# Kernel tuning notes

Hardware: AMD Instinct MI355X
Metric: run time of the kernel (lower is better)

The kernel has to match this reference:

```python
import jax, jax.numpy as jnp
import numpy as np
import itertools

B, G, FEAT, IMG = 2048, 8, 512, 1024
SCALES = list(range(G, 1, -1))  # [8,7,6,5,4,3,2]
SUBSAMPLE = 12


def setup_inputs() -> dict:
    key = jax.random.key(0)
    keys = jax.random.split(key, 1 + 2 * len(SCALES))
    rng = np.random.default_rng(0)
    inp = {"input": jax.random.normal(keys[0], (B, G, FEAT), dtype=jnp.float32)}
    for i, scale in enumerate(SCALES):
        perms = np.array(list(itertools.permutations(range(G), scale)), dtype=np.int32)
        n_sub = min(SUBSAMPLE, len(perms))
        sel = rng.choice(len(perms), n_sub, replace=False)
        inp[f"perms{i}"] = jnp.asarray(perms[sel])  # [n_sub, scale] int32
        lim = 1.0 / np.sqrt(scale * FEAT)
        inp[f"W{i}"] = jax.random.uniform(keys[1 + 2 * i], (IMG, scale * FEAT), minval=-lim, maxval=lim, dtype=jnp.float32)
        inp[f"b{i}"] = jax.random.uniform(keys[2 + 2 * i], (IMG,), minval=-lim, maxval=lim, dtype=jnp.float32)
    return inp


def _forward(input, perms_list, W_list, b_list):
    outs = []
    for perms, W, b in zip(perms_list, W_list, b_list):
        # gather: [B, n_sub, scale, FEAT] -> [B, n_sub, scale*FEAT]
        g = input[:, perms, :]
        g = g.reshape(g.shape[0], g.shape[1], -1)
        # batched linear over all subsamples, then mean over subsamples
        y = jnp.einsum('bsf,df->bsd', g, W) + b  # [B, n_sub, IMG]
        outs.append(y.mean(axis=1))
    return jnp.concatenate(outs, axis=1)  # [B, len(SCALES)*IMG]


def reference(input, perms0, W0, b0, perms1, W1, b1, perms2, W2, b2,
              perms3, W3, b3, perms4, W4, b4, perms5, W5, b5, perms6, W6, b6):
    perms_list = [perms0, perms1, perms2, perms3, perms4, perms5, perms6]
    W_list = [W0, W1, W2, W3, W4, W5, W6]
    b_list = [b0, b1, b2, b3, b4, b5, b6]
    return _forward(input, perms_list, W_list, b_list)
```

## Files before the change

kernel.cpp:

```cpp
#include <hip/hip_runtime.h>

typedef unsigned short u16;
typedef __bf16 bf16x8 __attribute__((ext_vector_type(8)));
typedef float f32x4 __attribute__((ext_vector_type(4)));

__device__ __forceinline__ u16 f2bf(float f) {
  unsigned int u = __float_as_uint(f);
  return (u16)((u + 0x7fffu + ((u >> 16) & 1u)) >> 16);
}

__device__ __forceinline__ int cumK(int i) { return 256 * i * (17 - i); }

__global__ __launch_bounds__(256) void k_xbar(
    const float* __restrict__ x,
    const int* p0, const int* p1, const int* p2, const int* p3,
    const int* p4, const int* p5, const int* p6,
    u16* __restrict__ Xb) {
  __shared__ float sc[448];
  const int b = blockIdx.x;
  const int t = threadIdx.x;
  const int* ps[7] = {p0, p1, p2, p3, p4, p5, p6};
  for (int cell = t; cell < 448; cell += 256) {
    int i = cell >> 6, rem = cell & 63, g = rem >> 3, j = rem & 7;
    int scale = 8 - i;
    float v = 0.f;
    if (j < scale) {
      const int* p = ps[i];
      int cnt = 0;
      for (int s = 0; s < 12; ++s) cnt += (p[s * scale + j] == g) ? 1 : 0;
      v = (float)cnt * (1.0f / 12.0f);
    }
    sc[cell] = v;
  }
  __syncthreads();
  const int u = t & 63;
  const int wv = t >> 6;
  const float4* xrow = reinterpret_cast<const float4*>(x + (size_t)b * 4096);
  float4 xr0[8], xr1[8];
#pragma unroll
  for (int g = 0; g < 8; ++g) {
    xr0[g] = xrow[g * 128 + u * 2];
    xr1[g] = xrow[g * 128 + u * 2 + 1];
  }
  u16* orow = Xb + (size_t)b * 17920;
  for (int s = wv; s < 35; s += 4) {
    int i = 0, rem = s;
    while (rem >= 8 - i) { rem -= 8 - i; ++i; }
    const int j = rem;
    float4 A0 = make_float4(0.f, 0.f, 0.f, 0.f);
    float4 A1 = make_float4(0.f, 0.f, 0.f, 0.f);
#pragma unroll
    for (int g = 0; g < 8; ++g) {
      const float c = sc[i * 64 + g * 8 + j];
      A0.x += c * xr0[g].x; A0.y += c * xr0[g].y;
      A0.z += c * xr0[g].z; A0.w += c * xr0[g].w;
      A1.x += c * xr1[g].x; A1.y += c * xr1[g].y;
      A1.z += c * xr1[g].z; A1.w += c * xr1[g].w;
    }
    uint4 o;
    o.x = (unsigned)f2bf(A0.x) | ((unsigned)f2bf(A0.y) << 16);
    o.y = (unsigned)f2bf(A0.z) | ((unsigned)f2bf(A0.w) << 16);
    o.z = (unsigned)f2bf(A1.x) | ((unsigned)f2bf(A1.y) << 16);
    o.w = (unsigned)f2bf(A1.z) | ((unsigned)f2bf(A1.w) << 16);
    *reinterpret_cast<uint4*>(orow + cumK(i) + j * 512 + u * 8) = o;
  }
}

__global__ __launch_bounds__(256) void k_wcast(
    const float* W0, const float* W1, const float* W2, const float* W3,
    const float* W4, const float* W5, const float* W6,
    u16* __restrict__ Wcat) {
  int i = 0, rem = blockIdx.x;
  while (rem >= (8 - i) * 512) { rem -= (8 - i) * 512; ++i; }
  const float* Wi = (i == 0) ? W0 : (i == 1) ? W1 : (i == 2) ? W2 :
                    (i == 3) ? W3 : (i == 4) ? W4 : (i == 5) ? W5 : W6;
  const int t = threadIdx.x;
  const float4 w = reinterpret_cast<const float4*>(Wi)[(size_t)rem * 256 + t];
  ushort4 o;
  o.x = f2bf(w.x); o.y = f2bf(w.y); o.z = f2bf(w.z); o.w = f2bf(w.w);
  reinterpret_cast<ushort4*>(Wcat + ((size_t)cumK(i) + rem) * 1024)[t] = o;
}

__device__ __forceinline__ void gl_lds16(const u16* g, u16* l) {
  __builtin_amdgcn_global_load_lds(
      (const __attribute__((address_space(1))) void*)g,
      (__attribute__((address_space(3))) void*)l, 16, 0, 0);
}

#define WAIT_VM8 0x0F78
#define WAIT_VM0 0x0F70

__global__ __launch_bounds__(256) void k_gemm_ms(
    const u16* __restrict__ Xb, const u16* __restrict__ Wcat,
    const float* b0, const float* b1, const float* b2, const float* b3,
    const float* b4, const float* b5, const float* b6,
    float* __restrict__ out) {
  __shared__ u16 lds[2 * 16384];
  const int i = blockIdx.x >> 7;
  const int s = blockIdx.x & 127;
  const int region = s & 7;
  const int k = s >> 3;
  const int mq = region >> 1;
  const int nq = region & 1;
  const int m0 = (mq * 4 + (k & 3)) * 128;
  const int n0loc = (nq * 4 + (k >> 2)) * 128;
  const int K = (8 - i) * 512;
  const int niter = K >> 6;
  const size_t baseB = (size_t)cumK(i) * 1024;

  const int tid = threadIdx.x;
  const int lane = tid & 63;
  const int wave = tid >> 6;
  const int quad = lane >> 4;
  const int l15 = lane & 15;
  const int waveM = (wave >> 1) * 64;
  const int waveN = (wave & 1) * 64;

  const int srow = tid >> 3;
  const int sslot = tid & 7;
  const int gch = (sslot - srow) & 7;
  const u16* pA0 = Xb + (size_t)(m0 + srow) * 17920 + cumK(i) + gch * 8;
  const u16* pB0 = Wcat + baseB + (size_t)(n0loc + srow) * K + gch * 8;
  const size_t strideAj = (size_t)32 * 17920;
  const size_t strideBj = (size_t)32 * K;
  u16* lA0 = lds + tid * 8;
  u16* lB0 = lds + 8192 + tid * 8;

  int offA[2][4], offB[2][4];
#pragma unroll
  for (int t = 0; t < 2; ++t) {
#pragma unroll
    for (int q = 0; q < 4; ++q) {
      int rowA = waveM + q * 16 + l15;
      offA[t][q] = rowA * 64 + (((t * 4 + quad) + rowA) & 7) * 8;
      int rowB = waveN + q * 16 + l15;
      offB[t][q] = 8192 + rowB * 64 + (((t * 4 + quad) + rowB) & 7) * 8;
    }
  }

  f32x4 acc[4][4];
#pragma unroll
  for (int q = 0; q < 4; ++q)
#pragma unroll
    for (int c = 0; c < 4; ++c) {
      f32x4 z = {0.f, 0.f, 0.f, 0.f};
      acc[q][c] = z;
    }

#pragma unroll
  for (int j = 0; j < 4; ++j) {
    gl_lds16(pA0 + j * strideAj, lA0 + j * 2048);
    gl_lds16(pB0 + j * strideBj, lB0 + j * 2048);
  }

  for (int kt = 0; kt < niter - 1; ++kt) {
    const size_t ko = (size_t)(kt + 1) * 64;
    const int nb = ((kt + 1) & 1) << 14;
#pragma unroll
    for (int j = 0; j < 4; ++j) {
      gl_lds16(pA0 + j * strideAj + ko, lA0 + nb + j * 2048);
      gl_lds16(pB0 + j * strideBj + ko, lB0 + nb + j * 2048);
    }
    __builtin_amdgcn_s_waitcnt(WAIT_VM8);
    __builtin_amdgcn_s_barrier();
    const int boff = (kt & 1) << 14;
#pragma unroll
    for (int t = 0; t < 2; ++t) {
      bf16x8 av[4], bv[4];
#pragma unroll
      for (int q = 0; q < 4; ++q) av[q] = *reinterpret_cast<const bf16x8*>(lds + boff + offA[t][q]);
#pragma unroll
      for (int c = 0; c < 4; ++c) bv[c] = *reinterpret_cast<const bf16x8*>(lds + boff + offB[t][c]);
#pragma unroll
      for (int q = 0; q < 4; ++q)
#pragma unroll
        for (int c = 0; c < 4; ++c)
          acc[q][c] = __builtin_amdgcn_mfma_f32_16x16x32_bf16(av[q], bv[c], acc[q][c], 0, 0, 0);
    }
    __builtin_amdgcn_s_barrier();
  }

  __builtin_amdgcn_s_waitcnt(WAIT_VM0);
  __builtin_amdgcn_s_barrier();
  {
    const int boff = ((niter - 1) & 1) << 14;
#pragma unroll
    for (int t = 0; t < 2; ++t) {
      bf16x8 av[4], bv[4];
#pragma unroll
      for (int q = 0; q < 4; ++q) av[q] = *reinterpret_cast<const bf16x8*>(lds + boff + offA[t][q]);
#pragma unroll
      for (int c = 0; c < 4; ++c) bv[c] = *reinterpret_cast<const bf16x8*>(lds + boff + offB[t][c]);
#pragma unroll
      for (int q = 0; q < 4; ++q)
#pragma unroll
        for (int c = 0; c < 4; ++c)
          acc[q][c] = __builtin_amdgcn_mfma_f32_16x16x32_bf16(av[q], bv[c], acc[q][c], 0, 0, 0);
    }
  }

  const float* bi = (i == 0) ? b0 : (i == 1) ? b1 : (i == 2) ? b2 :
                    (i == 3) ? b3 : (i == 4) ? b4 : (i == 5) ? b5 : b6;
#pragma unroll
  for (int c = 0; c < 4; ++c) {
    const int nloc = n0loc + waveN + c * 16 + l15;
    const float bias = bi[nloc];
    const int ncol = i * 1024 + nloc;
#pragma unroll
    for (int q = 0; q < 4; ++q) {
      const int mbase = m0 + waveM + q * 16 + quad * 4;
#pragma unroll
      for (int reg = 0; reg < 4; ++reg)
        out[(size_t)(mbase + reg) * 7168 + ncol] = acc[q][c][reg] + bias;
    }
  }
}

extern "C" void kernel_launch(void* const* d_in, const int* in_sizes, int n_in,
                              void* d_out, int out_size, void* d_ws, size_t ws_size,
                              hipStream_t stream) {
  const float* input = (const float*)d_in[0];
  const int* perms[7];
  const float* W[7];
  const float* bias[7];
  for (int i = 0; i < 7; ++i) {
    perms[i] = (const int*)d_in[1 + 3 * i];
    W[i]     = (const float*)d_in[2 + 3 * i];
    bias[i]  = (const float*)d_in[3 + 3 * i];
  }
  char* ws = (char*)d_ws;
  u16* Xb   = (u16*)ws;
  u16* Wcat = (u16*)(ws + (size_t)2048 * 17920 * 2);

  k_xbar<<<2048, 256, 0, stream>>>(input, perms[0], perms[1], perms[2], perms[3],
                                   perms[4], perms[5], perms[6], Xb);
  k_wcast<<<17920, 256, 0, stream>>>(W[0], W[1], W[2], W[3], W[4], W[5], W[6], Wcat);
  k_gemm_ms<<<896, 256, 0, stream>>>(Xb, Wcat,
                                     bias[0], bias[1], bias[2], bias[3],
                                     bias[4], bias[5], bias[6],
                                     (float*)d_out);
}
```

Before: 279.0 us.

## Halve GEMM K-tile to 32 to shrink LDS and raise occupancy; reorder scale blocks

The GEMM K-step drops from 64 to 32, which halves the LDS buffers from 64KB to 32KB and comes with a new 4-chunk swizzle for the shared-memory layout. launch_bounds now asks for 5 blocks per CU so more workgroups can be resident at once. Block-to-scale mapping is also reordered so long-K and short-K scales interleave across the grid, which is meant to balance load. The cost is twice as many barriers and waits per unit of K, with less MFMA work between each sync.

```diff
diff --git a/kernel.cpp b/kernel.cpp
--- a/kernel.cpp
+++ b/kernel.cpp
@@ -87,16 +87,18 @@
       (__attribute__((address_space(3))) void*)l, 16, 0, 0);
 }
 
-#define WAIT_VM8 0x0F78
+#define WAIT_VM4 0x0F74
 #define WAIT_VM0 0x0F70
 
-__global__ __launch_bounds__(256) void k_gemm_ms(
+__global__ __launch_bounds__(256, 5) void k_gemm_ms(
     const u16* __restrict__ Xb, const u16* __restrict__ Wcat,
     const float* b0, const float* b1, const float* b2, const float* b3,
     const float* b4, const float* b5, const float* b6,
     float* __restrict__ out) {
-  __shared__ u16 lds[2 * 16384];
-  const int i = blockIdx.x >> 7;
+  __shared__ u16 lds[2 * 8192];
+  const int r = blockIdx.x >> 7;
+  const int i = (r == 0) ? 0 : (r == 1) ? 1 : (r == 2) ? 4 :
+                (r == 3) ? 2 : (r == 4) ? 5 : (r == 5) ? 3 : 6;
   const int s = blockIdx.x & 127;
   const int region = s & 7;
   const int k = s >> 3;
@@ -105,7 +107,7 @@
   const int m0 = (mq * 4 + (k & 3)) * 128;
   const int n0loc = (nq * 4 + (k >> 2)) * 128;
   const int K = (8 - i) * 512;
-  const int niter = K >> 6;
+  const int niter = K >> 5;
   const size_t baseB = (size_t)cumK(i) * 1024;
 
   const int tid = threadIdx.x;
@@ -116,26 +118,22 @@
   const int waveM = (wave >> 1) * 64;
   const int waveN = (wave & 1) * 64;
 
-  const int srow = tid >> 3;
-  const int sslot = tid & 7;
-  const int gch = (sslot - srow) & 7;
+  const int srow = tid >> 2;
+  const int gch = ((tid & 3) - (tid >> 3)) & 3;
   const u16* pA0 = Xb + (size_t)(m0 + srow) * 17920 + cumK(i) + gch * 8;
   const u16* pB0 = Wcat + baseB + (size_t)(n0loc + srow) * K + gch * 8;
-  const size_t strideAj = (size_t)32 * 17920;
-  const size_t strideBj = (size_t)32 * K;
+  const size_t strideA2 = (size_t)64 * 17920;
+  const size_t strideB2 = (size_t)64 * K;
   u16* lA0 = lds + tid * 8;
-  u16* lB0 = lds + 8192 + tid * 8;
-
-  int offA[2][4], offB[2][4];
-#pragma unroll
-  for (int t = 0; t < 2; ++t) {
-#pragma unroll
-    for (int q = 0; q < 4; ++q) {
-      int rowA = waveM + q * 16 + l15;
-      offA[t][q] = rowA * 64 + (((t * 4 + quad) + rowA) & 7) * 8;
-      int rowB = waveN + q * 16 + l15;
-      offB[t][q] = 8192 + rowB * 64 + (((t * 4 + quad) + rowB) & 7) * 8;
-    }
+  u16* lB0 = lds + 4096 + tid * 8;
+
+  int offA[4], offB[4];
+#pragma unroll
+  for (int q = 0; q < 4; ++q) {
+    int rowA = waveM + q * 16 + l15;
+    offA[q] = rowA * 32 + ((quad + (rowA >> 1)) & 3) * 8;
+    int rowB = waveN + q * 16 + l15;
+    offB[q] = 4096 + rowB * 32 + ((quad + (rowB >> 1)) & 3) * 8;
   }
 
   f32x4 acc[4][4];
@@ -147,56 +145,48 @@
       acc[q][c] = z;
     }
 
-#pragma unroll
-  for (int j = 0; j < 4; ++j) {
-    gl_lds16(pA0 + j * strideAj, lA0 + j * 2048);
-    gl_lds16(pB0 + j * strideBj, lB0 + j * 2048);
-  }
+  gl_lds16(pA0, lA0);
+  gl_lds16(pA0 + strideA2, lA0 + 2048);
+  gl_lds16(pB0, lB0);
+  gl_lds16(pB0 + strideB2, lB0 + 2048);
 
   for (int kt = 0; kt < niter - 1; ++kt) {
-    const size_t ko = (size_t)(kt + 1) * 64;
-    const int nb = ((kt + 1) & 1) << 14;
-#pragma unroll
-    for (int j = 0; j < 4; ++j) {
-      gl_lds16(pA0 + j * strideAj + ko, lA0 + nb + j * 2048);
-      gl_lds16(pB0 + j * strideBj + ko, lB0 + nb + j * 2048);
-    }
-    __builtin_amdgcn_s_waitcnt(WAIT_VM8);
+    const size_t ko = (size_t)(kt + 1) * 32;
+    const int nb = ((kt + 1) & 1) << 13;
+    gl_lds16(pA0 + ko, lA0 + nb);
+    gl_lds16(pA0 + strideA2 + ko, lA0 + nb + 2048);
+    gl_lds16(pB0 + ko, lB0 + nb);
+    gl_lds16(pB0 + strideB2 + ko, lB0 + nb + 2048);
+    __builtin_amdgcn_s_waitcnt(WAIT_VM4);
     __builtin_amdgcn_s_barrier();
-    const int boff = (kt & 1) << 14;
-#pragma unroll
-    for (int t = 0; t < 2; ++t) {
-      bf16x8 av[4], bv[4];
-#pragma unroll
-      for (int q = 0; q < 4; ++q) av[q] = *reinterpret_cast<const bf16x8*>(lds + boff + offA[t][q]);
-#pragma unroll
-      for (int c = 0; c < 4; ++c) bv[c] = *reinterpret_cast<const bf16x8*>(lds + boff + offB[t][c]);
-#pragma unroll
-      for (int q = 0; q < 4; ++q)
-#pragma unroll
-        for (int c = 0; c < 4; ++c)
-          acc[q][c] = __builtin_amdgcn_mfma_f32_16x16x32_bf16(av[q], bv[c], acc[q][c], 0, 0, 0);
-    }
+    const int boff = (kt & 1) << 13;
+    bf16x8 av[4], bv[4];
+#pragma unroll
+    for (int q = 0; q < 4; ++q) av[q] = *reinterpret_cast<const bf16x8*>(lds + boff + offA[q]);
+#pragma unroll
+    for (int c = 0; c < 4; ++c) bv[c] = *reinterpret_cast<const bf16x8*>(lds + boff + offB[c]);
+#pragma unroll
+    for (int q = 0; q < 4; ++q)
+#pragma unroll
+      for (int c = 0; c < 4; ++c)
+        acc[q][c] = __builtin_amdgcn_mfma_f32_16x16x32_bf16(av[q], bv[c], acc[q][c], 0, 0, 0);
     __builtin_amdgcn_s_barrier();
   }
 
   __builtin_amdgcn_s_waitcnt(WAIT_VM0);
   __builtin_amdgcn_s_barrier();
   {
-    const int boff = ((niter - 1) & 1) << 14;
-#pragma unroll
-    for (int t = 0; t < 2; ++t) {
-      bf16x8 av[4], bv[4];
-#pragma unroll
-      for (int q = 0; q < 4; ++q) av[q] = *reinterpret_cast<const bf16x8*>(lds + boff + offA[t][q]);
-#pragma unroll
-      for (int c = 0; c < 4; ++c) bv[c] = *reinterpret_cast<const bf16x8*>(lds + boff + offB[t][c]);
-#pragma unroll
-      for (int q = 0; q < 4; ++q)
-#pragma unroll
-        for (int c = 0; c < 4; ++c)
-          acc[q][c] = __builtin_amdgcn_mfma_f32_16x16x32_bf16(av[q], bv[c], acc[q][c], 0, 0, 0);
-    }
+    const int boff = ((niter - 1) & 1) << 13;
+    bf16x8 av[4], bv[4];
+#pragma unroll
+    for (int q = 0; q < 4; ++q) av[q] = *reinterpret_cast<const bf16x8*>(lds + boff + offA[q]);
+#pragma unroll
+    for (int c = 0; c < 4; ++c) bv[c] = *reinterpret_cast<const bf16x8*>(lds + boff + offB[c]);
+#pragma unroll
+    for (int q = 0; q < 4; ++q)
+#pragma unroll
+      for (int c = 0; c < 4; ++c)
+        acc[q][c] = __builtin_amdgcn_mfma_f32_16x16x32_bf16(av[q], bv[c], acc[q][c], 0, 0, 0);
   }
 
   const float* bi = (i == 0) ? b0 : (i == 1) ? b1 : (i == 2) ? b2 :
```

Measured after the change: 305.2 us. 9.4% more time.

## Switch GEMM to 32x32x16 MFMA tiles and interleave scale block order

Applied to the files above, without the earlier changes.

Replaces the 16x16x32 bf16 MFMA tiling (a 4x4 grid of fragments per wave) with 32x32x16 MFMA (2x2 fragments per wave). This halves the LDS fragment reads per k-step and uses the larger matrix instruction, which has higher operand reuse. It also remaps block index to scale index so long-K and short-K scales are interleaved across the grid, which should balance the tail. The epilogue is rewritten for the 32x32 accumulator layout, and any mistake in the row/column mapping would give wrong outputs.

```diff
diff --git a/kernel.cpp b/kernel.cpp
--- a/kernel.cpp
+++ b/kernel.cpp
@@ -2,7 +2,7 @@
 
 typedef unsigned short u16;
 typedef __bf16 bf16x8 __attribute__((ext_vector_type(8)));
-typedef float f32x4 __attribute__((ext_vector_type(4)));
+typedef float f32x16 __attribute__((ext_vector_type(16)));
 
 __device__ __forceinline__ u16 f2bf(float f) {
   unsigned int u = __float_as_uint(f);
@@ -96,7 +96,9 @@
     const float* b4, const float* b5, const float* b6,
     float* __restrict__ out) {
   __shared__ u16 lds[2 * 16384];
-  const int i = blockIdx.x >> 7;
+  const int r = blockIdx.x >> 7;
+  const int i = (r == 0) ? 0 : (r == 1) ? 1 : (r == 2) ? 4 :
+                (r == 3) ? 2 : (r == 4) ? 5 : (r == 5) ? 3 : 6;
   const int s = blockIdx.x & 127;
   const int region = s & 7;
   const int k = s >> 3;
@@ -111,8 +113,8 @@
   const int tid = threadIdx.x;
   const int lane = tid & 63;
   const int wave = tid >> 6;
-  const int quad = lane >> 4;
-  const int l15 = lane & 15;
+  const int l31 = lane & 31;
+  const int half = lane >> 5;
   const int waveM = (wave >> 1) * 64;
   const int waveN = (wave & 1) * 64;
 
@@ -126,26 +128,24 @@
   u16* lA0 = lds + tid * 8;
   u16* lB0 = lds + 8192 + tid * 8;
 
-  int offA[2][4], offB[2][4];
-#pragma unroll
-  for (int t = 0; t < 2; ++t) {
-#pragma unroll
-    for (int q = 0; q < 4; ++q) {
-      int rowA = waveM + q * 16 + l15;
-      offA[t][q] = rowA * 64 + (((t * 4 + quad) + rowA) & 7) * 8;
-      int rowB = waveN + q * 16 + l15;
-      offB[t][q] = 8192 + rowB * 64 + (((t * 4 + quad) + rowB) & 7) * 8;
-    }
-  }
-
-  f32x4 acc[4][4];
-#pragma unroll
-  for (int q = 0; q < 4; ++q)
-#pragma unroll
-    for (int c = 0; c < 4; ++c) {
-      f32x4 z = {0.f, 0.f, 0.f, 0.f};
-      acc[q][c] = z;
-    }
+  int offA[4][2], offB[4][2];
+#pragma unroll
+  for (int kk = 0; kk < 4; ++kk) {
+#pragma unroll
+    for (int f = 0; f < 2; ++f) {
+      int rowA = waveM + f * 32 + l31;
+      offA[kk][f] = rowA * 64 + (((kk * 2 + half) + rowA) & 7) * 8;
+      int rowB = waveN + f * 32 + l31;
+      offB[kk][f] = 8192 + rowB * 64 + (((kk * 2 + half) + rowB) & 7) * 8;
+    }
+  }
+
+  f32x16 acc[2][2];
+#pragma unroll
+  for (int q = 0; q < 2; ++q)
+#pragma unroll
+    for (int c = 0; c < 2; ++c)
+      acc[q][c] = (f32x16)(0.f);
 
 #pragma unroll
   for (int j = 0; j < 4; ++j) {
@@ -165,17 +165,18 @@
     __builtin_amdgcn_s_barrier();
     const int boff = (kt & 1) << 14;
 #pragma unroll
-    for (int t = 0; t < 2; ++t) {
-      bf16x8 av[4], bv[4];
-#pragma unroll
-      for (int q = 0; q < 4; ++q) av[q] = *reinterpret_cast<const bf16x8*>(lds + boff + offA[t][q]);
-#pragma unroll
-      for (int c = 0; c < 4; ++c) bv[c] = *reinterpret_cast<const bf16x8*>(lds + boff + offB[t][c]);
-#pragma unroll
-      for (int q = 0; q < 4; ++q)
-#pragma unroll
-        for (int c = 0; c < 4; ++c)
-          acc[q][c] = __builtin_amdgcn_mfma_f32_16x16x32_bf16(av[q], bv[c], acc[q][c], 0, 0, 0);
+    for (int kk = 0; kk < 4; ++kk) {
+      bf16x8 av[2], bv[2];
+#pragma unroll
+      for (int f = 0; f < 2; ++f) {
+        av[f] = *reinterpret_cast<const bf16x8*>(lds + boff + offA[kk][f]);
+        bv[f] = *reinterpret_cast<const bf16x8*>(lds + boff + offB[kk][f]);
+      }
+#pragma unroll
+      for (int q = 0; q < 2; ++q)
+#pragma unroll
+        for (int c = 0; c < 2; ++c)
+          acc[q][c] = __builtin_amdgcn_mfma_f32_32x32x16_bf16(av[q], bv[c], acc[q][c], 0, 0, 0);
     }
     __builtin_amdgcn_s_barrier();
   }
@@ -185,33 +186,36 @@
   {
     const int boff = ((niter - 1) & 1) << 14;
 #pragma unroll
-    for (int t = 0; t < 2; ++t) {
-      bf16x8 av[4], bv[4];
-#pragma unroll
-      for (int q = 0; q < 4; ++q) av[q] = *reinterpret_cast<const bf16x8*>(lds + boff + offA[t][q]);
-#pragma unroll
-      for (int c = 0; c < 4; ++c) bv[c] = *reinterpret_cast<const bf16x8*>(lds + boff + offB[t][c]);
-#pragma unroll
-      for (int q = 0; q < 4; ++q)
-#pragma unroll
-        for (int c = 0; c < 4; ++c)
-          acc[q][c] = __builtin_amdgcn_mfma_f32_16x16x32_bf16(av[q], bv[c], acc[q][c], 0, 0, 0);
+    for (int kk = 0; kk < 4; ++kk) {
+      bf16x8 av[2], bv[2];
+#pragma unroll
+      for (int f = 0; f < 2; ++f) {
+        av[f] = *reinterpret_cast<const bf16x8*>(lds + boff + offA[kk][f]);
+        bv[f] = *reinterpret_cast<const bf16x8*>(lds + boff + offB[kk][f]);
+      }
+#pragma unroll
+      for (int q = 0; q < 2; ++q)
+#pragma unroll
+        for (int c = 0; c < 2; ++c)
+          acc[q][c] = __builtin_amdgcn_mfma_f32_32x32x16_bf16(av[q], bv[c], acc[q][c], 0, 0, 0);
     }
   }
 
   const float* bi = (i == 0) ? b0 : (i == 1) ? b1 : (i == 2) ? b2 :
                     (i == 3) ? b3 : (i == 4) ? b4 : (i == 5) ? b5 : b6;
 #pragma unroll
-  for (int c = 0; c < 4; ++c) {
-    const int nloc = n0loc + waveN + c * 16 + l15;
+  for (int c = 0; c < 2; ++c) {
+    const int nloc = n0loc + waveN + c * 32 + l31;
     const float bias = bi[nloc];
     const int ncol = i * 1024 + nloc;
 #pragma unroll
-    for (int q = 0; q < 4; ++q) {
-      const int mbase = m0 + waveM + q * 16 + quad * 4;
-#pragma unroll
-      for (int reg = 0; reg < 4; ++reg)
-        out[(size_t)(mbase + reg) * 7168 + ncol] = acc[q][c][reg] + bias;
+    for (int q = 0; q < 2; ++q) {
+      const int mbase = m0 + waveM + q * 32 + 4 * half;
+#pragma unroll
+      for (int reg = 0; reg < 16; ++reg) {
+        const int row = mbase + (reg & 3) + 8 * (reg >> 2);
+        out[(size_t)row * 7168 + ncol] = acc[q][c][reg] + bias;
+      }
     }
   }
 }
```

Result: slower. 290.4 us (+4.1%).
